# Optimization experiments

Hardware: AMD Instinct MI355X
Metric: run time of the kernel (lower is better)

## Reference

```python
import jax, jax.numpy as jnp
import numpy as np

CHANNELS = 64
K = 3
STRIDE = 1
GROUP_CHANNELS = 2
GROUPS = CHANNELS // GROUP_CHANNELS  # 32
RED = 4
PAD = (K - 1) // 2


def setup_inputs() -> dict:
    key = jax.random.key(0)
    ks = jax.random.split(key, 6)
    x = jax.random.normal(ks[0], (8, CHANNELS, 128, 128), dtype=jnp.float32)
    w1 = jax.random.normal(ks[1], (CHANNELS // RED, CHANNELS), dtype=jnp.float32) * 0.05
    b1 = jax.random.normal(ks[2], (CHANNELS // RED,), dtype=jnp.float32) * 0.05
    prelu_a = jnp.full((1,), 0.25, dtype=jnp.float32)
    w2 = jax.random.normal(ks[3], (K * K * GROUPS, CHANNELS // RED), dtype=jnp.float32) * 0.05
    b2 = jax.random.normal(ks[4], (K * K * GROUPS,), dtype=jnp.float32) * 0.05
    return {"x": x, "w1": w1, "b1": b1, "prelu_a": prelu_a, "w2": w2, "b2": b2}


def reference(x, w1, b1, prelu_a, w2, b2):
    # stride == 1: no avgpool
    # 1x1 conv -> PReLU -> 1x1 conv to generate per-pixel kernels
    t = jnp.einsum('bchw,oc->bohw', x, w1) + b1[None, :, None, None]
    t = jnp.where(t >= 0, t, prelu_a[0] * t)  # PReLU, single shared slope
    weight = jnp.einsum('bchw,oc->bohw', t, w2) + b2[None, :, None, None]
    b, _, h, w = weight.shape
    # (b, groups, 1, k^2, h, w)
    weight = weight.reshape(b, GROUPS, 1, K * K, h, w)
    # unfold: im2col with padding 1, stride 1; channel-major (c, kh, kw) ordering like torch.nn.Unfold
    xp = jnp.pad(x, ((0, 0), (0, 0), (PAD, PAD), (PAD, PAD)))
    patches = jnp.stack(
        [xp[:, :, i:i + h, j:j + w] for i in range(K) for j in range(K)], axis=2
    )  # (b, c, k^2, h, w)
    patches = patches.reshape(b, GROUPS, GROUP_CHANNELS, K * K, h, w)
    out = (weight * patches).sum(axis=3).reshape(b, CHANNELS, h, w)
    return out
```

## Files before the change

### kernel.cpp

```cpp
#include <hip/hip_runtime.h>

#define NPIX (128 * 128)
#define CH 64
#define RMID 16
#define KK 9
#define TOTPIX (8 * NPIX)
#define PLANE_B 65536

typedef float v2f __attribute__((ext_vector_type(2)));

__global__ __launch_bounds__(256) void conv1_kernel(
    const float* __restrict__ x,
    const float* __restrict__ w1,
    const float* __restrict__ b1,
    const float* __restrict__ prelu_a,
    float* __restrict__ t_ws)
{
    __shared__ v2f pl[4][64][17];

    const int c     = threadIdx.x & 63;
    const int layer = threadIdx.x >> 6;

    const int L     = blockIdx.x;
    const int bq    = L & 7;
    const int chunk = L >> 3;
    const int p0    = chunk * 128 + 2 * c;
    const int G0    = (bq << 14) + p0;

    const float* xp = x + (size_t)bq * CH * NPIX + (size_t)(16 * layer) * NPIX + p0;

    v2f xv[16];
#pragma unroll
    for (int k = 0; k < 16; ++k) xv[k] = *(const v2f*)(xp + (size_t)k * NPIX);

    v2f t2[RMID];
#pragma unroll
    for (int r = 0; r < RMID; ++r) {
        const float b = (layer == 0) ? b1[r] : 0.f;
        t2[r].x = b; t2[r].y = b;
    }

#pragma unroll
    for (int k = 0; k < 16; ++k) {
#pragma unroll
        for (int r = 0; r < RMID; ++r) {
            const float w = w1[r * CH + 16 * layer + k];
            v2f wv; wv.x = w; wv.y = w;
            t2[r] = __builtin_elementwise_fma(wv, xv[k], t2[r]);
        }
    }
#pragma unroll
    for (int r = 0; r < RMID; ++r) pl[layer][c][r] = t2[r];
    __syncthreads();

    const float a  = prelu_a[0];
    const int   r0 = 4 * layer;
    float s0[4], s1[4];
#pragma unroll
    for (int i = 0; i < 4; ++i) {
        const v2f v = pl[0][c][r0 + i] + pl[1][c][r0 + i]
                    + pl[2][c][r0 + i] + pl[3][c][r0 + i];
        s0[i] = (v.x >= 0.f) ? v.x : a * v.x;
        s1[i] = (v.y >= 0.f) ? v.y : a * v.y;
    }
    float* tb = t_ws + (size_t)G0 * 16 + r0;
    *(float4*)(tb)      = make_float4(s0[0], s0[1], s0[2], s0[3]);
    *(float4*)(tb + 16) = make_float4(s1[0], s1[1], s1[2], s1[3]);
}

__global__ __launch_bounds__(256) void invol_kernel(
    const float* __restrict__ x,
    const float* __restrict__ t_ws,
    const float* __restrict__ w2,
    const float* __restrict__ b2,
    float* __restrict__ out)
{
    const int c    = threadIdx.x & 63;
    const int rsub = threadIdx.x >> 6;

    const int L     = blockIdx.x;
    const int bq    = L & 7;
    const int gp    = (L >> 3) & 15;
    const int strip = L >> 7;

    const int hq  = 4 * strip + rsub;
    const int p0  = hq * 128 + 2 * c;
    const int G0  = (bq << 14) + p0;
    const int pb0 = 4 * p0;

    const v2f* tb = (const v2f*)(t_ws + (size_t)G0 * 16);
    v2f trA[8], trB[8];
#pragma unroll
    for (int i = 0; i < 8; ++i) { trA[i] = tb[i]; trB[i] = tb[8 + i]; }

    const float rm0 = (hq > 0)   ? 1.f : 0.f;
    const float rm2 = (hq < 127) ? 1.f : 0.f;
    const float mL  = (c > 0)    ? 1.f : 0.f;
    const float mR  = (c < 63)   ? 1.f : 0.f;
    const int   ro0 = (hq > 0)   ? -512 : 0;
    const int   ro2 = (hq < 127) ?  512 : 0;

    const char* xbc = (const char*)(x + (size_t)bq * CH * NPIX);
    char*       obc = (char*)(out + (size_t)bq * CH * NPIX);

#pragma unroll
    for (int gi = 0; gi < 2; ++gi) {
        const int g = 2 * gp + gi;
        const char* cp0 = xbc + (size_t)(2 * g) * PLANE_B;
        const char* cp1 = cp0 + PLANE_B;

        v2f A0 = *(const v2f*)(cp0 + (size_t)(pb0 + ro0));
        v2f A1 = *(const v2f*)(cp0 + (size_t)pb0);
        v2f A2 = *(const v2f*)(cp0 + (size_t)(pb0 + ro2));
        v2f E0 = *(const v2f*)(cp1 + (size_t)(pb0 + ro0));
        v2f E1 = *(const v2f*)(cp1 + (size_t)pb0);
        v2f E2 = *(const v2f*)(cp1 + (size_t)(pb0 + ro2));

        v2f wgp[KK];
#pragma unroll
        for (int k = 0; k < KK; ++k) {
            const v2f* w2r2 = (const v2f*)(w2 + (g * KK + k) * RMID);
            v2f accA, accB;
            accA.x = b2[g * KK + k]; accA.y = 0.f;
            accB = accA;
#pragma unroll
            for (int r = 0; r < RMID / 2; ++r) {
                accA = __builtin_elementwise_fma(w2r2[r], trA[r], accA);
                accB = __builtin_elementwise_fma(w2r2[r], trB[r], accB);
            }
            wgp[k].x = accA.x + accA.y;
            wgp[k].y = accB.x + accB.y;
        }
        wgp[0].x *= mL;  wgp[3].x *= mL;  wgp[6].x *= mL;
        wgp[2].y *= mR;  wgp[5].y *= mR;  wgp[8].y *= mR;
        { v2f r0v; r0v.x = rm0; r0v.y = rm0;  A0 *= r0v;  E0 *= r0v; }
        { v2f r2v; r2v.x = rm2; r2v.y = rm2;  A2 *= r2v;  E2 *= r2v; }

        const float lA0 = __shfl_up(A0.y, 1), rA0 = __shfl_down(A0.x, 1);
        const float lA1 = __shfl_up(A1.y, 1), rA1 = __shfl_down(A1.x, 1);
        const float lA2 = __shfl_up(A2.y, 1), rA2 = __shfl_down(A2.x, 1);
        const float lE0 = __shfl_up(E0.y, 1), rE0 = __shfl_down(E0.x, 1);
        const float lE1 = __shfl_up(E1.y, 1), rE1 = __shfl_down(E1.x, 1);
        const float lE2 = __shfl_up(E2.y, 1), rE2 = __shfl_down(E2.x, 1);

        v2f oA; oA.x = 0.f; oA.y = 0.f;
        v2f oB = oA;
        v2f tp;
        tp.x = lA0;  tp.y = A0.x;  oA = __builtin_elementwise_fma(wgp[0], tp, oA);
                                    oA = __builtin_elementwise_fma(wgp[1], A0, oA);
        tp.x = A0.y; tp.y = rA0;   oA = __builtin_elementwise_fma(wgp[2], tp, oA);
        tp.x = lA1;  tp.y = A1.x;  oA = __builtin_elementwise_fma(wgp[3], tp, oA);
                                    oA = __builtin_elementwise_fma(wgp[4], A1, oA);
        tp.x = A1.y; tp.y = rA1;   oA = __builtin_elementwise_fma(wgp[5], tp, oA);
        tp.x = lA2;  tp.y = A2.x;  oA = __builtin_elementwise_fma(wgp[6], tp, oA);
                                    oA = __builtin_elementwise_fma(wgp[7], A2, oA);
        tp.x = A2.y; tp.y = rA2;   oA = __builtin_elementwise_fma(wgp[8], tp, oA);

        tp.x = lE0;  tp.y = E0.x;  oB = __builtin_elementwise_fma(wgp[0], tp, oB);
                                    oB = __builtin_elementwise_fma(wgp[1], E0, oB);
        tp.x = E0.y; tp.y = rE0;   oB = __builtin_elementwise_fma(wgp[2], tp, oB);
        tp.x = lE1;  tp.y = E1.x;  oB = __builtin_elementwise_fma(wgp[3], tp, oB);
                                    oB = __builtin_elementwise_fma(wgp[4], E1, oB);
        tp.x = E1.y; tp.y = rE1;   oB = __builtin_elementwise_fma(wgp[5], tp, oB);
        tp.x = lE2;  tp.y = E2.x;  oB = __builtin_elementwise_fma(wgp[6], tp, oB);
                                    oB = __builtin_elementwise_fma(wgp[7], E2, oB);
        tp.x = E2.y; tp.y = rE2;   oB = __builtin_elementwise_fma(wgp[8], tp, oB);

        __builtin_nontemporal_store(oA, (v2f*)(obc + (size_t)(2 * g)     * PLANE_B + pb0));
        __builtin_nontemporal_store(oB, (v2f*)(obc + (size_t)(2 * g + 1) * PLANE_B + pb0));
    }
}

extern "C" void kernel_launch(void* const* d_in, const int* in_sizes, int n_in,
                              void* d_out, int out_size, void* d_ws, size_t ws_size,
                              hipStream_t stream)
{
    const float* x  = (const float*)d_in[0];
    const float* w1 = (const float*)d_in[1];
    const float* b1 = (const float*)d_in[2];
    const float* pa = (const float*)d_in[3];
    const float* w2 = (const float*)d_in[4];
    const float* b2 = (const float*)d_in[5];
    float* out  = (float*)d_out;
    float* t_ws = (float*)d_ws;

    hipLaunchKernelGGL(conv1_kernel, dim3(1024), dim3(256), 0, stream,
                       x, w1, b1, pa, t_ws);
    hipLaunchKernelGGL(invol_kernel, dim3(4096), dim3(256), 0, stream,
                       x, t_ws, w2, b2, out);
}
```

Baseline: 123.2 us.

## Fuse conv1 reduction into involution kernel, recomputing hidden features per block

Merges the 1x1 conv + PReLU kernel into the involution kernel. Each thread now computes the 16 hidden features for its two pixels directly from all 64 input channels and keeps them in registers, so the t workspace write/read and the second launch go away. Each block now handles 8 groups instead of 2, so the grid shrinks to 1024 blocks. Four blocks per pixel strip each redo the full 64-channel conv1, which adds x reads and FMAs. Per-thread register pressure also rises.

```diff
diff --git a/kernel.cpp b/kernel.cpp
--- a/kernel.cpp
+++ b/kernel.cpp
@@ -4,73 +4,15 @@
 #define CH 64
 #define RMID 16
 #define KK 9
-#define TOTPIX (8 * NPIX)
 #define PLANE_B 65536
 
 typedef float v2f __attribute__((ext_vector_type(2)));
 
-__global__ __launch_bounds__(256) void conv1_kernel(
+__global__ __launch_bounds__(256) void invol_fused(
     const float* __restrict__ x,
     const float* __restrict__ w1,
     const float* __restrict__ b1,
     const float* __restrict__ prelu_a,
-    float* __restrict__ t_ws)
-{
-    __shared__ v2f pl[4][64][17];
-
-    const int c     = threadIdx.x & 63;
-    const int layer = threadIdx.x >> 6;
-
-    const int L     = blockIdx.x;
-    const int bq    = L & 7;
-    const int chunk = L >> 3;
-    const int p0    = chunk * 128 + 2 * c;
-    const int G0    = (bq << 14) + p0;
-
-    const float* xp = x + (size_t)bq * CH * NPIX + (size_t)(16 * layer) * NPIX + p0;
-
-    v2f xv[16];
-#pragma unroll
-    for (int k = 0; k < 16; ++k) xv[k] = *(const v2f*)(xp + (size_t)k * NPIX);
-
-    v2f t2[RMID];
-#pragma unroll
-    for (int r = 0; r < RMID; ++r) {
-        const float b = (layer == 0) ? b1[r] : 0.f;
-        t2[r].x = b; t2[r].y = b;
-    }
-
-#pragma unroll
-    for (int k = 0; k < 16; ++k) {
-#pragma unroll
-        for (int r = 0; r < RMID; ++r) {
-            const float w = w1[r * CH + 16 * layer + k];
-            v2f wv; wv.x = w; wv.y = w;
-            t2[r] = __builtin_elementwise_fma(wv, xv[k], t2[r]);
-        }
-    }
-#pragma unroll
-    for (int r = 0; r < RMID; ++r) pl[layer][c][r] = t2[r];
-    __syncthreads();
-
-    const float a  = prelu_a[0];
-    const int   r0 = 4 * layer;
-    float s0[4], s1[4];
-#pragma unroll
-    for (int i = 0; i < 4; ++i) {
-        const v2f v = pl[0][c][r0 + i] + pl[1][c][r0 + i]
-                    + pl[2][c][r0 + i] + pl[3][c][r0 + i];
-        s0[i] = (v.x >= 0.f) ? v.x : a * v.x;
-        s1[i] = (v.y >= 0.f) ? v.y : a * v.y;
-    }
-    float* tb = t_ws + (size_t)G0 * 16 + r0;
-    *(float4*)(tb)      = make_float4(s0[0], s0[1], s0[2], s0[3]);
-    *(float4*)(tb + 16) = make_float4(s1[0], s1[1], s1[2], s1[3]);
-}
-
-__global__ __launch_bounds__(256) void invol_kernel(
-    const float* __restrict__ x,
-    const float* __restrict__ t_ws,
     const float* __restrict__ w2,
     const float* __restrict__ b2,
     float* __restrict__ out)
@@ -80,18 +22,50 @@
 
     const int L     = blockIdx.x;
     const int bq    = L & 7;
-    const int gp    = (L >> 3) & 15;
-    const int strip = L >> 7;
+    const int go    = (L >> 3) & 3;
+    const int strip = L >> 5;
 
     const int hq  = 4 * strip + rsub;
     const int p0  = hq * 128 + 2 * c;
-    const int G0  = (bq << 14) + p0;
     const int pb0 = 4 * p0;
 
-    const v2f* tb = (const v2f*)(t_ws + (size_t)G0 * 16);
-    v2f trA[8], trB[8];
+    const float* xb  = x + (size_t)bq * CH * NPIX;
+    const char*  xbc = (const char*)xb;
+
+    v2f t2[RMID];
 #pragma unroll
-    for (int i = 0; i < 8; ++i) { trA[i] = tb[i]; trB[i] = tb[8 + i]; }
+    for (int r = 0; r < RMID; ++r) {
+        const float b = b1[r];
+        t2[r].x = b; t2[r].y = b;
+    }
+    const float* xp = xb + p0;
+#pragma unroll
+    for (int cc = 0; cc < CH; cc += 8) {
+        v2f xv[8];
+#pragma unroll
+        for (int k = 0; k < 8; ++k)
+            xv[k] = *(const v2f*)(xp + (size_t)(cc + k) * NPIX);
+#pragma unroll
+        for (int k = 0; k < 8; ++k) {
+#pragma unroll
+            for (int r = 0; r < RMID; ++r) {
+                const float w = w1[r * CH + cc + k];
+                v2f wv; wv.x = w; wv.y = w;
+                t2[r] = __builtin_elementwise_fma(wv, xv[k], t2[r]);
+            }
+        }
+    }
+    {
+        const float a = prelu_a[0];
+        v2f av; av.x = a; av.y = a;
+        v2f z;  z.x = 0.f; z.y = 0.f;
+#pragma unroll
+        for (int r = 0; r < RMID; ++r) {
+            const v2f pos = __builtin_elementwise_max(t2[r], z);
+            const v2f neg = __builtin_elementwise_min(t2[r], z);
+            t2[r] = __builtin_elementwise_fma(av, neg, pos);
+        }
+    }
 
     const float rm0 = (hq > 0)   ? 1.f : 0.f;
     const float rm2 = (hq < 127) ? 1.f : 0.f;
@@ -100,12 +74,11 @@
     const int   ro0 = (hq > 0)   ? -512 : 0;
     const int   ro2 = (hq < 127) ?  512 : 0;
 
-    const char* xbc = (const char*)(x + (size_t)bq * CH * NPIX);
-    char*       obc = (char*)(out + (size_t)bq * CH * NPIX);
+    char* obc = (char*)(out + (size_t)bq * CH * NPIX);
 
 #pragma unroll
-    for (int gi = 0; gi < 2; ++gi) {
-        const int g = 2 * gp + gi;
+    for (int gi = 0; gi < 8; ++gi) {
+        const int g = 8 * go + gi;
         const char* cp0 = xbc + (size_t)(2 * g) * PLANE_B;
         const char* cp1 = cp0 + PLANE_B;
 
@@ -119,17 +92,16 @@
         v2f wgp[KK];
 #pragma unroll
         for (int k = 0; k < KK; ++k) {
-            const v2f* w2r2 = (const v2f*)(w2 + (g * KK + k) * RMID);
-            v2f accA, accB;
-            accA.x = b2[g * KK + k]; accA.y = 0.f;
-            accB = accA;
+            const float* w2r = w2 + (g * KK + k) * RMID;
+            const float bb = b2[g * KK + k];
+            v2f acc; acc.x = bb; acc.y = bb;
 #pragma unroll
-            for (int r = 0; r < RMID / 2; ++r) {
-                accA = __builtin_elementwise_fma(w2r2[r], trA[r], accA);
-                accB = __builtin_elementwise_fma(w2r2[r], trB[r], accB);
+            for (int r = 0; r < RMID; ++r) {
+                const float w = w2r[r];
+                v2f wv; wv.x = w; wv.y = w;
+                acc = __builtin_elementwise_fma(wv, t2[r], acc);
             }
-            wgp[k].x = accA.x + accA.y;
-            wgp[k].y = accB.x + accB.y;
+            wgp[k] = acc;
         }
         wgp[0].x *= mL;  wgp[3].x *= mL;  wgp[6].x *= mL;
         wgp[2].y *= mR;  wgp[5].y *= mR;  wgp[8].y *= mR;
@@ -181,11 +153,8 @@
     const float* pa = (const float*)d_in[3];
     const float* w2 = (const float*)d_in[4];
     const float* b2 = (const float*)d_in[5];
-    float* out  = (float*)d_out;
-    float* t_ws = (float*)d_ws;
+    float* out = (float*)d_out;
 
-    hipLaunchKernelGGL(conv1_kernel, dim3(1024), dim3(256), 0, stream,
-                       x, w1, b1, pa, t_ws);
-    hipLaunchKernelGGL(invol_kernel, dim3(4096), dim3(256), 0, stream,
-                       x, t_ws, w2, b2, out);
+    hipLaunchKernelGGL(invol_fused, dim3(1024), dim3(256), 0, stream,
+                       x, w1, b1, pa, w2, b2, out);
 }
```

Result: no change. 121.1 us (-1.7%).
